# Kernel optimization log

Hardware: AMD Instinct MI355X
Metric: run time of the kernel (lower is better)

The kernel has to match this reference:

```python
import jax, jax.numpy as jnp
import numpy as np

B, L = 2, 1024
D_MODEL, D_CKV, D_CQ = 1024, 256, 512
N_HEAD, D_HEAD, D_ROPE = 8, 64, 32
N_IDX_HEAD = 4
K_TS, LW = 96, 64
ROPE_BASE = 10000.0


def setup_inputs() -> dict:
    key = jax.random.key(0)
    ks = jax.random.split(key, 14)
    def w(k, shape, fan_in):
        return jax.random.normal(k, shape, dtype=jnp.float32) * (fan_in ** -0.5)
    return {
        "x": jax.random.normal(ks[0], (B, L, D_MODEL), dtype=jnp.float32),
        "W_dkv": w(ks[1], (D_MODEL, D_CKV), D_MODEL),
        "W_uk": w(ks[2], (D_CKV, N_HEAD * D_HEAD), D_CKV),
        "W_uv": w(ks[3], (D_CKV, N_HEAD * D_HEAD), D_CKV),
        "W_dq": w(ks[4], (D_MODEL, D_CQ), D_MODEL),
        "W_uq": w(ks[5], (D_CQ, N_HEAD * D_HEAD), D_CQ),
        "W_qr": w(ks[6], (D_CQ, N_HEAD * D_ROPE), D_CQ),
        "W_kr": w(ks[7], (D_MODEL, D_ROPE), D_MODEL),
        "W_out": w(ks[8], (N_HEAD * D_HEAD, D_MODEL), N_HEAD * D_HEAD),
        "idx_wq": w(ks[9], (D_MODEL, N_IDX_HEAD * D_HEAD), D_MODEL),
        "idx_wk": w(ks[10], (D_MODEL, D_HEAD), D_MODEL),
        "idx_w": jnp.ones((N_IDX_HEAD,), dtype=jnp.float32),
        "raw_delta": jax.random.normal(ks[11], (D_ROPE // 2,), dtype=jnp.float32) * 0.1,
    }


def _pope(x, angles):
    # PoPE: softplus -> chunk in half -> rotate by (base_angle + learned delta)
    cos, sin = jnp.cos(angles), jnp.sin(angles)
    mu1, mu2 = jnp.split(jax.nn.softplus(x), 2, axis=-1)
    return jnp.concatenate([mu1 * cos - mu2 * sin, mu1 * sin + mu2 * cos], axis=-1)


def _forward(x, W_dkv, W_uk, W_uv, W_dq, W_uq, W_qr, W_kr, W_out,
             idx_wq, idx_wk, idx_w, raw_delta):
    B_, L_, _ = x.shape
    c_kv = x @ W_dkv                                    # [B,L,d_ckv]

    # ---- LightningIndexer ----
    q_i = (x @ idx_wq).reshape(B_, L_, N_IDX_HEAD, D_HEAD)
    k_i = x @ idx_wk                                    # [B,L,D_HEAD]
    s_i = jax.nn.relu(jnp.einsum('bthd,bsd->bths', q_i, k_i))
    I = jnp.einsum('bths,h->bts', s_i, idx_w)           # [B,L,L]

    # ---- TokenSelector (local window forced in, causal masked out, top-k) ----
    qpos = jnp.arange(L_)[:, None]
    kpos = jnp.arange(L_)[None, :]
    local = (kpos >= qpos - LW + 1) & (kpos <= qpos)
    causal = kpos > qpos
    I = jnp.where(local[None], jnp.inf, I)
    I = jnp.where(causal[None], -jnp.inf, I)
    kk = min(K_TS, L_)
    _, idx = jax.lax.top_k(I, kk)                       # [B,L,kk] int32

    bi = jnp.arange(B_)[:, None, None]
    # gather-after-project (per-token linear => identical math, far less memory)
    key_c = (c_kv @ W_uk)[bi, idx].reshape(B_, L_, kk, N_HEAD, D_HEAD)
    value = (c_kv @ W_uv)[bi, idx].reshape(B_, L_, kk, N_HEAD, D_HEAD)

    c_q = x @ W_dq                                      # [B,L,d_cq]
    query_c = (c_q @ W_uq).reshape(B_, L_, N_HEAD, D_HEAD)

    # ---- PoPE angles ----
    half = D_ROPE // 2
    theta = 1.0 / ROPE_BASE ** (2.0 * jnp.arange(half, dtype=jnp.float32) / D_ROPE)
    delta = -2.0 * jnp.pi * jax.nn.sigmoid(raw_delta)   # [half]
    angles_q = jnp.arange(L_, dtype=jnp.float32)[:, None] * theta[None, :] + delta  # [L,half]
    query_r = _pope((c_q @ W_qr).reshape(B_, L_, N_HEAD, D_ROPE),
                    angles_q[None, :, None, :])         # [B,L,H,D_ROPE]

    # key_r: PoPE applied along the selected-slot axis (faithful to original permute)
    kr_sel = (x @ W_kr)[bi, idx]                        # [B,L,kk,D_ROPE]
    angles_k = jnp.arange(kk, dtype=jnp.float32)[:, None] * theta[None, :] + delta  # [kk,half]
    key_r = _pope(kr_sel, angles_k[None, None, :, :])   # [B,L,kk,D_ROPE]

    # ---- per-query sparse attention ----
    scale = (D_HEAD + D_ROPE) ** (-0.5)
    q_c = query_c.transpose(0, 2, 1, 3)                 # [B,H,L,d]
    q_r = query_r.transpose(0, 2, 1, 3)                 # [B,H,L,dr]
    k_c = key_c.transpose(0, 3, 1, 2, 4)                # [B,H,L,kk,d]
    v = value.transpose(0, 3, 1, 2, 4)                  # [B,H,L,kk,d]
    scores = (jnp.einsum('bhld,bhlkd->bhlk', q_c, k_c)
              + jnp.einsum('bhld,blkd->bhlk', q_r, key_r)) * scale
    attn = jax.nn.softmax(scores.astype(jnp.float32), axis=-1).astype(v.dtype)
    out = jnp.einsum('bhlk,bhlkd->bhld', attn, v)       # [B,H,L,d]
    out = out.transpose(0, 2, 1, 3).reshape(B_, L_, N_HEAD * D_HEAD)
    return out @ W_out


def reference(x, W_dkv, W_uk, W_uv, W_dq, W_uq, W_qr, W_kr, W_out,
              idx_wq, idx_wk, idx_w, raw_delta):
    return _forward(x, W_dkv, W_uk, W_uv, W_dq, W_uq, W_qr, W_kr, W_out,
                    idx_wq, idx_wk, idx_w, raw_delta)
```

## Files before the change

### kernel.cpp

```cpp
#include <hip/hip_runtime.h>
#include <math.h>

typedef unsigned short u16;
typedef unsigned int u32;
typedef unsigned long long u64;
typedef _Float16 f16;
typedef __attribute__((ext_vector_type(8))) _Float16 f16x8;
typedef __attribute__((ext_vector_type(4))) float f32x4;

#define L      1024
#define NH     8
#define DH     64
#define DR     32
#define KTS    96
#define LWIN   64
#define NKV    1024
#define NQP    768

__device__ __forceinline__ float softplusf(float x) {
  return fmaxf(x, 0.f) + log1pf(expf(-fabsf(x)));
}
__device__ __forceinline__ f32x4 mf16(f16x8 a, f16x8 b, f32x4 c) {
  return __builtin_amdgcn_mfma_f32_16x16x32_f16(a, b, c, 0, 0, 0);
}
__device__ __forceinline__ u64 pack4(u16 a, u16 b, u16 c, u16 d) {
  return (u64)a | ((u64)b << 16) | ((u64)c << 32) | ((u64)d << 48);
}
__device__ __forceinline__ u64 umax64(u64 a, u64 b) { return a > b ? a : b; }
__device__ __forceinline__ void f16split(float x, u16& h, u16& l) {
  f16 hh = (f16)x;
  float r = x - (float)hh;
  f16 ll = (f16)r;
  h = *(u16*)&hh; l = *(u16*)&ll;
}
__device__ __forceinline__ u16 f16bits(float x) {
  f16 hh = (f16)x;
  return *(u16*)&hh;
}

struct TSrc { const float* p; int n0, w; };
struct WJob { TSrc s0, s1, s2, s3, s4; int K; u16 *Ph, *Pl; int nbx, nby; };

__global__ __launch_bounds__(256) void wsplit4(WJob j0, WJob j1, WJob j2,
                                               WJob j3) {
  __shared__ float tile[32][33];
  WJob j = (blockIdx.z == 0) ? j0
         : (blockIdx.z == 1) ? j1
         : (blockIdx.z == 2) ? j2 : j3;
  if ((int)blockIdx.x >= j.nbx || (int)blockIdx.y >= j.nby) return;
  const int k0 = blockIdx.y * 32, n0 = blockIdx.x * 32;
  const int tid = threadIdx.x;
  const float* sp = nullptr; int off = 0, w = 0;
  if (j.s0.p && n0 >= j.s0.n0 && n0 < j.s0.n0 + j.s0.w) { sp = j.s0.p; off = j.s0.n0; w = j.s0.w; }
  else if (j.s1.p && n0 >= j.s1.n0 && n0 < j.s1.n0 + j.s1.w) { sp = j.s1.p; off = j.s1.n0; w = j.s1.w; }
  else if (j.s2.p && n0 >= j.s2.n0 && n0 < j.s2.n0 + j.s2.w) { sp = j.s2.p; off = j.s2.n0; w = j.s2.w; }
  else if (j.s3.p && n0 >= j.s3.n0 && n0 < j.s3.n0 + j.s3.w) { sp = j.s3.p; off = j.s3.n0; w = j.s3.w; }
  else if (j.s4.p && n0 >= j.s4.n0 && n0 < j.s4.n0 + j.s4.w) { sp = j.s4.p; off = j.s4.n0; w = j.s4.w; }
  {
    const int kl = tid >> 3, n4 = (tid & 7) * 4;
    float4 v = make_float4(0.f, 0.f, 0.f, 0.f);
    if (sp) v = *(const float4*)(sp + (size_t)(k0 + kl) * w + (n0 - off) + n4);
    tile[kl][n4 + 0] = v.x; tile[kl][n4 + 1] = v.y;
    tile[kl][n4 + 2] = v.z; tile[kl][n4 + 3] = v.w;
  }
  __syncthreads();
  const int nl = tid >> 3, k4 = (tid & 7) * 4;
  u16 h[4], lo[4];
#pragma unroll
  for (int q = 0; q < 4; ++q) f16split(tile[k4 + q][nl], h[q], lo[q]);
  const size_t o = (size_t)(n0 + nl) * j.K + k0 + k4;
  *(u64*)(j.Ph + o) = pack4(h[0], h[1], h[2], h[3]);
  *(u64*)(j.Pl + o) = pack4(lo[0], lo[1], lo[2], lo[3]);
}

__global__ __launch_bounds__(256) void xsplit(
    const float* __restrict__ x, u16* __restrict__ Xh, u16* __restrict__ Xl) {
  const int i = (blockIdx.x * 256 + threadIdx.x) * 4;
  float4 v = *(const float4*)(x + i);
  float e[4] = {v.x, v.y, v.z, v.w};
  u16 h[4], lo[4];
#pragma unroll
  for (int j = 0; j < 4; ++j) f16split(e[j], h[j], lo[j]);
  *(u64*)(Xh + i) = pack4(h[0], h[1], h[2], h[3]);
  *(u64*)(Xl + i) = pack4(lo[0], lo[1], lo[2], lo[3]);
}

struct GArg {
  const u16 *A0, *A1, *B0, *B1;
  float* C; u16* Ch;
  u16 *Qh, *Ql, *Kh, *Kl; float* KR; const float* IW;
  int lda, ldc, K, nbn;
};

template <int NPROD, int OUT>
__device__ __forceinline__ void gemm_body(const GArg& g, u16* Al, u16* Bl) {
  const int NS = (NPROD == 1) ? 1 : 2;
  const int tid = threadIdx.x;
  const int l = tid & 63, w = tid >> 6;
  const int wr = w >> 1, wc = w & 1;
  const int l15 = l & 15, l4 = l >> 4;
  const int bm = blockIdx.y * 128, bn = blockIdx.x * 128;
  const int ar2 = tid >> 1, akc = (tid & 1) * 16;
  const int brr = tid >> 2, bkc = (tid & 3) * 8;

  f32x4 acc[4][4];
#pragma unroll
  for (int i = 0; i < 4; ++i)
#pragma unroll
    for (int j = 0; j < 4; ++j) acc[i][j] = (f32x4){0.f, 0.f, 0.f, 0.f};

  for (int k0 = 0; k0 < g.K; k0 += 32) {
#pragma unroll
    for (int p = 0; p < NS; ++p) {
      const u16* Ap = (p == 0) ? g.A0 : g.A1;
      const size_t ab = (size_t)(bm + ar2) * g.lda + k0 + akc;
      *(uint4*)&Al[p * 5120 + ar2 * 40 + akc] = *(const uint4*)(Ap + ab);
      *(uint4*)&Al[p * 5120 + ar2 * 40 + akc + 8] = *(const uint4*)(Ap + ab + 8);
      const u16* Bp = (p == 0) ? g.B0 : g.B1;
#pragma unroll
      for (int i = 0; i < 2; ++i) {
        const int row = brr + i * 64;
        *(uint4*)&Bl[p * 5120 + row * 40 + bkc] =
            *(const uint4*)(Bp + (size_t)(bn + row) * g.K + k0 + bkc);
      }
    }
    __syncthreads();
    f16x8 af[NS == 1 ? 1 : 2][4], bf[NS == 1 ? 1 : 2][4];
#pragma unroll
    for (int f = 0; f < 4; ++f) {
      const int arow = wr * 64 + f * 16 + l15;
      const int brow = wc * 64 + f * 16 + l15;
#pragma unroll
      for (int p = 0; p < NS; ++p) {
        af[p][f] = *(const f16x8*)&Al[p * 5120 + arow * 40 + l4 * 8];
        bf[p][f] = *(const f16x8*)&Bl[p * 5120 + brow * 40 + l4 * 8];
      }
    }
#pragma unroll
    for (int fm = 0; fm < 4; ++fm)
#pragma unroll
      for (int fn = 0; fn < 4; ++fn) {
        f32x4 c = acc[fm][fn];
        c = mf16(af[0][fm], bf[0][fn], c);
        if (NPROD == 3) {
          c = mf16(af[0][fm], bf[1][fn], c);
          c = mf16(af[1][fm], bf[0][fn], c);
        }
        acc[fm][fn] = c;
      }
    __syncthreads();
  }
  if (OUT == 3) {
    const float w0 = g.IW[0], w1 = g.IW[1], w2 = g.IW[2], w3 = g.IW[3];
#pragma unroll
    for (int fm = 0; fm < 4; ++fm) {
      const int tt = (bm >> 2) + wr * 16 + fm * 4 + l4;
#pragma unroll
      for (int fn = 0; fn < 4; ++fn) {
        const int col = bn + wc * 64 + fn * 16 + l15;
        const f32x4 a = acc[fm][fn];
        float v = w0 * fmaxf(a[0], 0.f) + w1 * fmaxf(a[1], 0.f)
                + w2 * fmaxf(a[2], 0.f) + w3 * fmaxf(a[3], 0.f);
        g.C[(size_t)tt * g.ldc + col] = v;
      }
    }
    return;
  }
#pragma unroll
  for (int fm = 0; fm < 4; ++fm)
#pragma unroll
    for (int j = 0; j < 4; ++j) {
      const int row = bm + wr * 64 + fm * 16 + l4 * 4 + j;
#pragma unroll
      for (int fn = 0; fn < 4; ++fn) {
        const int col = bn + wc * 64 + fn * 16 + l15;
        const float val = acc[fm][fn][j];
        if (OUT == 0) {
          g.C[(size_t)row * g.ldc + col] = val;
        } else if (OUT == 1) {
          g.Ch[(size_t)row * g.ldc + col] = f16bits(val);
        } else {
          u16 hh, ll;
          f16split(val, hh, ll);
          if (col < 256) {
            const size_t o = ((size_t)row * 4 + (col >> 6)) * 64 + (col & 63);
            g.Qh[o] = hh; g.Ql[o] = ll;
          } else if (col < 320) {
            const size_t o = (size_t)row * 64 + (col - 256);
            g.Kh[o] = hh; g.Kl[o] = ll;
          } else if (col < 352) {
            g.KR[(size_t)row * 32 + (col - 320)] = val;
          }
        }
      }
    }
}

template <int NPROD, int OUT>
__global__ __launch_bounds__(256) void mfma_gemm(GArg g0, GArg g1) {
  __shared__ u16 Al[(NPROD == 1 ? 1 : 2) * 5120];
  __shared__ u16 Bl[(NPROD == 1 ? 1 : 2) * 5120];
  GArg g = (blockIdx.z == 0) ? g0 : g1;
  if ((int)blockIdx.x >= g.nbn) return;
  gemm_body<NPROD, OUT>(g, Al, Bl);
}

__global__ __launch_bounds__(256) void g1_fused(GArg ga, GArg gb) {
  __shared__ u16 Al[2 * 5120];
  __shared__ u16 Bl[2 * 5120];
  if (blockIdx.z == 0) {
    if ((int)blockIdx.x >= ga.nbn) return;
    gemm_body<1, 1>(ga, Al, Bl);
  } else {
    if ((int)blockIdx.x >= gb.nbn) return;
    gemm_body<3, 2>(gb, Al, Bl);
  }
}

__global__ __launch_bounds__(256) void mid_fused(GArg gi0, GArg gi1, GArg g2,
                                                GArg g3) {
  __shared__ u16 Al[2 * 5120];
  __shared__ u16 Bl[2 * 5120];
  const int z = blockIdx.z;
  if (z < 2) {
    const GArg& g = z ? gi1 : gi0;
    if ((int)blockIdx.x >= g.nbn) return;
    gemm_body<3, 3>(g, Al, Bl);
  } else {
    const GArg& g = (z == 2) ? g2 : g3;
    if ((int)blockIdx.x >= g.nbn || (int)blockIdx.y >= 16) return;
    gemm_body<1, 0>(g, Al, Bl);
  }
}

__global__ __launch_bounds__(256) void topk2(
    const float* __restrict__ IM, int* __restrict__ idx_sel) {
  const int wave = threadIdx.x >> 6, lane = threadIdx.x & 63;
  const int bt = blockIdx.x * 4 + wave;
  const int b = bt >> 10, t = bt & 1023;
  int* out = idx_sel + (size_t)bt * KTS;
  if (t < LWIN) {
    out[lane] = lane;
    if (lane < 32) out[64 + lane] = 64 + lane;
    return;
  }
  out[lane] = t - 63 + lane;
  const int nf = t - 63;
  const float* Irow = IM + ((size_t)b << 20) + ((size_t)t << 10);
  u64 key[16];
#pragma unroll
  for (int gq = 0; gq < 4; ++gq) {
    const int s0 = gq * 256 + lane * 4;
    float4 v = make_float4(0.f, 0.f, 0.f, 0.f);
    if (s0 < nf) v = *(const float4*)(Irow + s0);
    float e[4] = {v.x, v.y, v.z, v.w};
#pragma unroll
    for (int c = 0; c < 4; ++c) {
      u64 k = 0ull;
      const int s = s0 + c;
      if (s < nf) {
        unsigned ib = __float_as_uint(e[c]);
        if (ib == 0x80000000u) ib = 0u;
        ib = (ib & 0x80000000u) ? ~ib : (ib | 0x80000000u);
        k = ((u64)ib << 32) | (u64)(0xFFFFFFFFu - (unsigned)s);
      }
      key[gq * 4 + c] = k;
    }
  }
  u64 lm = key[0];
#pragma unroll
  for (int j = 1; j < 16; ++j) lm = umax64(lm, key[j]);
  const int topM = nf < 32 ? nf : 32;
  for (int it = 0; it < topM; ++it) {
    u64 m = lm;
#pragma unroll
    for (int off = 32; off > 0; off >>= 1) m = umax64(m, __shfl_xor(m, off));
    if (lane == 0)
      out[64 + it] = (int)(0xFFFFFFFFu - (unsigned)(m & 0xFFFFFFFFull));
    if (lm == m) {
#pragma unroll
      for (int j = 0; j < 16; ++j)
        if (key[j] == m) key[j] = 0ull;
      lm = key[0];
#pragma unroll
      for (int j = 1; j < 16; ++j) lm = umax64(lm, key[j]);
    }
  }
  if (lane < 32 - topM) out[64 + topM + lane] = t + 1 + lane;
}

__global__ __launch_bounds__(256) void attn_kernel(
    const float* __restrict__ qproj, const float* __restrict__ kvproj,
    const float* __restrict__ krc, const int* __restrict__ idx_sel,
    const float* __restrict__ raw_delta, u16* __restrict__ aoh) {
  const int bt = ((blockIdx.x & 7) << 8) | (blockIdx.x >> 3);
  const int b = bt >> 10;
  const int t = bt & 1023;
  const int tid = threadIdx.x;

  __shared__ __align__(16) float qcs[NH * DH];
  __shared__ __align__(16) float qrs[NH * DR];
  __shared__ __align__(16) float krs[KTS * DR];
  __shared__ float scS[NH * 100];
  __shared__ int selS[KTS];
  __shared__ int offS[KTS];
  __shared__ float thetav[16], deltav[16];
  __shared__ float mu[NH * DR];

  const float* qrow = qproj + (size_t)bt * NQP;
  qcs[tid] = qrow[tid];
  qcs[256 + tid] = qrow[256 + tid];
  mu[tid] = softplusf(qrow[512 + tid]);
  if (tid < KTS) {
    int s = idx_sel[(size_t)bt * KTS + tid];
    selS[tid] = s;
    offS[tid] = s * NKV;
  }
  if (tid < 16) {
    thetav[tid] = (float)(1.0 / pow(10000.0, (double)tid / 16.0));
    float r = raw_delta[tid];
    deltav[tid] = -6.2831853071795864769f * (1.f / (1.f + expf(-r)));
  }
  __syncthreads();

  if (tid < 128) {
    int h = tid >> 4, i = tid & 15;
    float ang = (float)t * thetav[i] + deltav[i];
    float c = cosf(ang), s = sinf(ang);
    float m1 = mu[h * DR + i], m2 = mu[h * DR + 16 + i];
    qrs[h * DR + i] = m1 * c - m2 * s;
    qrs[h * DR + 16 + i] = m1 * s + m2 * c;
  }
  const float* krb = krc + (size_t)b * L * 32;
  for (int e = tid; e < KTS * 16; e += 256) {
    int k = e >> 4, i = e & 15;
    int s = selS[k];
    float x1 = krb[(size_t)s * 32 + i];
    float x2 = krb[(size_t)s * 32 + 16 + i];
    float m1 = softplusf(x1), m2 = softplusf(x2);
    float ang = (float)k * thetav[i] + deltav[i];
    float c = cosf(ang), sn = sinf(ang);
    krs[k * DR + i] = m1 * c - m2 * sn;
    krs[k * DR + 16 + i] = m1 * sn + m2 * c;
  }
  __syncthreads();

  const float scale = 0.10206207261596575f;
  const int h = tid >> 5;
  const int l = tid & 31;
  const float2 qv = *(const float2*)&qcs[h * DH + 2 * l];
  const float qr1 = qrs[h * DR + l];
  const float* kvb = kvproj + (size_t)b * L * NKV;
#pragma unroll 8
  for (int k = 0; k < KTS; ++k) {
    const float2 kv = *(const float2*)(kvb + offS[k] + 2 * tid);
    float p = qv.x * kv.x + qv.y * kv.y + qr1 * krs[k * DR + l];
#pragma unroll
    for (int off = 16; off > 0; off >>= 1) p += __shfl_xor(p, off, 32);
    if (l == 0) scS[h * 100 + k] = p * scale;
  }
  __syncthreads();

  {
    float s0 = scS[h * 100 + l], s1 = scS[h * 100 + l + 32],
          s2 = scS[h * 100 + l + 64];
    float mx = fmaxf(fmaxf(s0, s1), s2);
#pragma unroll
    for (int off = 16; off > 0; off >>= 1) mx = fmaxf(mx, __shfl_xor(mx, off, 32));
    float e0 = expf(s0 - mx), e1 = expf(s1 - mx), e2 = expf(s2 - mx);
    float sum = e0 + e1 + e2;
#pragma unroll
    for (int off = 16; off > 0; off >>= 1) sum += __shfl_xor(sum, off, 32);
    float inv = 1.f / sum;
    scS[h * 100 + l] = e0 * inv;
    scS[h * 100 + l + 32] = e1 * inv;
    scS[h * 100 + l + 64] = e2 * inv;
  }
  __syncthreads();

  float2 acc = make_float2(0.f, 0.f);
#pragma unroll 4
  for (int k = 0; k < KTS; ++k) {
    const float2 v = *(const float2*)(kvb + offS[k] + 512 + 2 * tid);
    const float w = scS[h * 100 + k];
    acc.x += w * v.x;
    acc.y += w * v.y;
  }
  const size_t o = (size_t)bt * 512 + 2 * tid;
  *(u32*)(aoh + o) = (u32)f16bits(acc.x) | ((u32)f16bits(acc.y) << 16);
}

extern "C" void kernel_launch(void* const* d_in, const int* in_sizes, int n_in,
                              void* d_out, int out_size, void* d_ws, size_t ws_size,
                              hipStream_t stream) {
  const float* x      = (const float*)d_in[0];
  const float* W_dkv  = (const float*)d_in[1];
  const float* W_uk   = (const float*)d_in[2];
  const float* W_uv   = (const float*)d_in[3];
  const float* W_dq   = (const float*)d_in[4];
  const float* W_uq   = (const float*)d_in[5];
  const float* W_qr   = (const float*)d_in[6];
  const float* W_kr   = (const float*)d_in[7];
  const float* W_out  = (const float*)d_in[8];
  const float* idx_wq = (const float*)d_in[9];
  const float* idx_wk = (const float*)d_in[10];
  const float* idx_w  = (const float*)d_in[11];
  const float* raw_dl = (const float*)d_in[12];
  float* out = (float*)d_out;

  const int M = 2 * L;
  u16* BxT_h  = (u16*)d_ws;
  u16* BxT_l  = BxT_h + 1152 * 1024;
  u16* BkvT_h = BxT_l + 1152 * 1024;
  u16* BkvT_l = BkvT_h + 1024 * 256;
  u16* BqT_h  = BkvT_l + 1024 * 256;
  u16* BqT_l  = BqT_h + 768 * 512;
  u16* WoT_h  = BqT_l + 768 * 512;
  u16* WoT_l  = WoT_h + 1024 * 512;
  u16* Xh     = WoT_l + 1024 * 512;
  u16* Xl     = Xh + (size_t)M * 1024;
  u16* XPh    = Xl + (size_t)M * 1024;
  u16* AOh    = XPh + (size_t)M * 768;
  u16* Qih    = AOh + (size_t)M * 512;
  u16* Qil    = Qih + (size_t)M * 4 * 64;
  u16* Kih    = Qil + (size_t)M * 4 * 64;
  u16* Kil    = Kih + (size_t)M * 64;
  float* krc    = (float*)(Kil + (size_t)M * 64);
  float* kvproj = krc + (size_t)M * 32;
  float* qproj  = kvproj + (size_t)M * NKV;
  int* sel      = (int*)(qproj + (size_t)M * NQP);
  float* IM     = (float*)Xh;

  dim3 blk(256);
  TSrc z = {nullptr, 0, 0};
  GArg Z = {};
  {
    WJob j0 = {{W_dkv, 0, 256}, {W_dq, 256, 512}, {idx_wq, 768, 256},
               {idx_wk, 1024, 64}, {W_kr, 1088, 32},
               1024, BxT_h, BxT_l, 36, 32};
    WJob j1 = {{W_uk, 0, 512}, {W_uv, 512, 512}, z, z, z,
               256, BkvT_h, BkvT_l, 32, 8};
    WJob j2 = {{W_uq, 0, 512}, {W_qr, 512, 256}, z, z, z,
               512, BqT_h, BqT_l, 24, 16};
    WJob j3 = {{W_out, 0, 1024}, z, z, z, z,
               512, WoT_h, WoT_l, 32, 16};
    hipLaunchKernelGGL(wsplit4, dim3(36, 32, 4), blk, 0, stream, j0, j1, j2, j3);
  }
  hipLaunchKernelGGL(xsplit, dim3(M * 1024 / (256 * 4)), blk, 0, stream,
                     x, Xh, Xl);
  {
    GArg ga = Z;
    ga.A0 = Xh; ga.B0 = BxT_h;
    ga.Ch = XPh; ga.lda = 1024; ga.ldc = 768; ga.K = 1024; ga.nbn = 6;
    GArg gb = Z;
    gb.A0 = Xh; gb.A1 = Xl;
    gb.B0 = BxT_h + 768 * 1024; gb.B1 = BxT_l + 768 * 1024;
    gb.Qh = Qih; gb.Ql = Qil; gb.Kh = Kih; gb.Kl = Kil; gb.KR = krc;
    gb.lda = 1024; gb.ldc = 0; gb.K = 1024; gb.nbn = 3;
    hipLaunchKernelGGL(g1_fused, dim3(6, M / 128, 2), blk, 0, stream, ga, gb);
  }
  {
    GArg gi0 = Z, gi1 = Z, g2 = Z, g3 = Z;
    gi0.A0 = Qih; gi0.A1 = Qil; gi0.B0 = Kih; gi0.B1 = Kil;
    gi0.C = IM; gi0.IW = idx_w;
    gi0.lda = 64; gi0.ldc = 1024; gi0.K = 64; gi0.nbn = 8;
    gi1 = gi0;
    gi1.A0 = Qih + 4096 * 64; gi1.A1 = Qil + 4096 * 64;
    gi1.B0 = Kih + 1024 * 64; gi1.B1 = Kil + 1024 * 64;
    gi1.C = IM + 1024 * 1024;
    g2.A0 = XPh; g2.B0 = BkvT_h;
    g2.C = kvproj; g2.lda = 768; g2.ldc = 1024; g2.K = 256; g2.nbn = 8;
    g3.A0 = XPh + 256; g3.B0 = BqT_h;
    g3.C = qproj; g3.lda = 768; g3.ldc = 768; g3.K = 512; g3.nbn = 6;
    hipLaunchKernelGGL(mid_fused, dim3(8, 32, 4), blk, 0, stream,
                       gi0, gi1, g2, g3);
  }
  hipLaunchKernelGGL(topk2, dim3(M / 4), blk, 0, stream, IM, sel);
  hipLaunchKernelGGL(attn_kernel, dim3(M), blk, 0, stream,
                     qproj, kvproj, krc, sel, raw_dl, AOh);
  {
    GArg g = Z;
    g.A0 = AOh; g.B0 = WoT_h;
    g.C = out; g.lda = 512; g.ldc = 1024; g.K = 512; g.nbn = 8;
    hipLaunchKernelGGL((mfma_gemm<1, 0>), dim3(8, M / 128, 1), blk, 0, stream,
                       g, g);
  }
}
```

Baseline: 283.8 us.

## Store attention keys in fp16 and use packed dot2 with batched shuffle reduction

The kv projection GEMM now writes the key half as fp16 and the value half as fp32 into separate buffers. The attention kernel gathers fp16 keys, which halves the bytes per selected key, and computes the score with the fdot2 instruction. The shuffle reduction now handles four keys at once through a butterfly transpose, cutting the number of shuffles per key. The cost is reduced key precision (fp16 queries and keys) in the score computation.

```diff
diff --git a/kernel.cpp b/kernel.cpp
--- a/kernel.cpp
+++ b/kernel.cpp
@@ -5,6 +5,7 @@
 typedef unsigned int u32;
 typedef unsigned long long u64;
 typedef _Float16 f16;
+typedef __attribute__((ext_vector_type(2))) _Float16 f16x2;
 typedef __attribute__((ext_vector_type(8))) _Float16 f16x8;
 typedef __attribute__((ext_vector_type(4))) float f32x4;
 
@@ -14,7 +15,6 @@
 #define DR     32
 #define KTS    96
 #define LWIN   64
-#define NKV    1024
 #define NQP    768
 
 __device__ __forceinline__ float softplusf(float x) {
@@ -36,6 +36,11 @@
 __device__ __forceinline__ u16 f16bits(float x) {
   f16 hh = (f16)x;
   return *(u16*)&hh;
+}
+__device__ __forceinline__ float fdot2u(u32 a, u32 b, float c) {
+  union { u32 u; f16x2 h; } ua, ub;
+  ua.u = a; ub.u = b;
+  return __builtin_amdgcn_fdot2(ua.h, ub.h, c, false);
 }
 
 struct TSrc { const float* p; int n0, w; };
@@ -179,6 +184,9 @@
           g.C[(size_t)row * g.ldc + col] = val;
         } else if (OUT == 1) {
           g.Ch[(size_t)row * g.ldc + col] = f16bits(val);
+        } else if (OUT == 4) {
+          if (col < 512) g.Ch[(size_t)row * 512 + col] = f16bits(val);
+          else g.C[(size_t)row * 512 + (col - 512)] = val;
         } else {
           u16 hh, ll;
           f16split(val, hh, ll);
@@ -226,10 +234,12 @@
     const GArg& g = z ? gi1 : gi0;
     if ((int)blockIdx.x >= g.nbn) return;
     gemm_body<3, 3>(g, Al, Bl);
+  } else if (z == 2) {
+    if ((int)blockIdx.x >= g2.nbn || (int)blockIdx.y >= 16) return;
+    gemm_body<1, 4>(g2, Al, Bl);
   } else {
-    const GArg& g = (z == 2) ? g2 : g3;
-    if ((int)blockIdx.x >= g.nbn || (int)blockIdx.y >= 16) return;
-    gemm_body<1, 0>(g, Al, Bl);
+    if ((int)blockIdx.x >= g3.nbn || (int)blockIdx.y >= 16) return;
+    gemm_body<1, 0>(g3, Al, Bl);
   }
 }
 
@@ -290,17 +300,18 @@
 }
 
 __global__ __launch_bounds__(256) void attn_kernel(
-    const float* __restrict__ qproj, const float* __restrict__ kvproj,
-    const float* __restrict__ krc, const int* __restrict__ idx_sel,
-    const float* __restrict__ raw_delta, u16* __restrict__ aoh) {
+    const float* __restrict__ qproj, const u16* __restrict__ kcf,
+    const float* __restrict__ vc, const float* __restrict__ krc,
+    const int* __restrict__ idx_sel, const float* __restrict__ raw_delta,
+    u16* __restrict__ aoh) {
   const int bt = ((blockIdx.x & 7) << 8) | (blockIdx.x >> 3);
   const int b = bt >> 10;
   const int t = bt & 1023;
   const int tid = threadIdx.x;
 
-  __shared__ __align__(16) float qcs[NH * DH];
   __shared__ __align__(16) float qrs[NH * DR];
   __shared__ __align__(16) float krs[KTS * DR];
+  __shared__ u32 qc2S[256];
   __shared__ float scS[NH * 100];
   __shared__ int selS[KTS];
   __shared__ int offS[KTS];
@@ -308,13 +319,16 @@
   __shared__ float mu[NH * DR];
 
   const float* qrow = qproj + (size_t)bt * NQP;
-  qcs[tid] = qrow[tid];
-  qcs[256 + tid] = qrow[256 + tid];
+  {
+    const int hh = tid >> 5, ll = tid & 31;
+    float q0 = qrow[hh * 64 + 2 * ll], q1 = qrow[hh * 64 + 2 * ll + 1];
+    qc2S[tid] = (u32)f16bits(q0) | ((u32)f16bits(q1) << 16);
+  }
   mu[tid] = softplusf(qrow[512 + tid]);
   if (tid < KTS) {
     int s = idx_sel[(size_t)bt * KTS + tid];
     selS[tid] = s;
-    offS[tid] = s * NKV;
+    offS[tid] = s * 512;
   }
   if (tid < 16) {
     thetav[tid] = (float)(1.0 / pow(10000.0, (double)tid / 16.0));
@@ -348,16 +362,30 @@
   const float scale = 0.10206207261596575f;
   const int h = tid >> 5;
   const int l = tid & 31;
-  const float2 qv = *(const float2*)&qcs[h * DH + 2 * l];
+  const u32 q2 = qc2S[tid];
   const float qr1 = qrs[h * DR + l];
-  const float* kvb = kvproj + (size_t)b * L * NKV;
-#pragma unroll 8
-  for (int k = 0; k < KTS; ++k) {
-    const float2 kv = *(const float2*)(kvb + offS[k] + 2 * tid);
-    float p = qv.x * kv.x + qv.y * kv.y + qr1 * krs[k * DR + l];
-#pragma unroll
-    for (int off = 16; off > 0; off >>= 1) p += __shfl_xor(p, off, 32);
-    if (l == 0) scS[h * 100 + k] = p * scale;
+  const u16* kcb = kcf + (size_t)b * L * 512 + h * 64 + 2 * l;
+  const float* vcb = vc + (size_t)b * L * 512;
+
+#pragma unroll 4
+  for (int i = 0; i < KTS / 4; ++i) {
+    const int kb = i * 4;
+    u32 kv0 = *(const u32*)(kcb + offS[kb + 0]);
+    u32 kv1 = *(const u32*)(kcb + offS[kb + 1]);
+    u32 kv2 = *(const u32*)(kcb + offS[kb + 2]);
+    u32 kv3 = *(const u32*)(kcb + offS[kb + 3]);
+    float p0 = fdot2u(q2, kv0, qr1 * krs[(kb + 0) * DR + l]);
+    float p1 = fdot2u(q2, kv1, qr1 * krs[(kb + 1) * DR + l]);
+    float p2 = fdot2u(q2, kv2, qr1 * krs[(kb + 2) * DR + l]);
+    float p3 = fdot2u(q2, kv3, qr1 * krs[(kb + 3) * DR + l]);
+    float a = ((l & 16) ? p1 : p0) + __shfl_xor((l & 16) ? p0 : p1, 16, 32);
+    float bb = ((l & 16) ? p3 : p2) + __shfl_xor((l & 16) ? p2 : p3, 16, 32);
+    float c = ((l & 8) ? bb : a) + __shfl_xor((l & 8) ? a : bb, 8, 32);
+    c += __shfl_xor(c, 4, 32);
+    c += __shfl_xor(c, 2, 32);
+    c += __shfl_xor(c, 1, 32);
+    if ((l & 7) == 0)
+      scS[h * 100 + kb + ((l >> 4) & 1) + ((l >> 3) & 1) * 2] = c * scale;
   }
   __syncthreads();
 
@@ -381,7 +409,7 @@
   float2 acc = make_float2(0.f, 0.f);
 #pragma unroll 4
   for (int k = 0; k < KTS; ++k) {
-    const float2 v = *(const float2*)(kvb + offS[k] + 512 + 2 * tid);
+    const float2 v = *(const float2*)(vcb + offS[k] + 2 * tid);
     const float w = scS[h * 100 + k];
     acc.x += w * v.x;
     acc.y += w * v.y;
@@ -425,9 +453,10 @@
   u16* Qil    = Qih + (size_t)M * 4 * 64;
   u16* Kih    = Qil + (size_t)M * 4 * 64;
   u16* Kil    = Kih + (size_t)M * 64;
-  float* krc    = (float*)(Kil + (size_t)M * 64);
-  float* kvproj = krc + (size_t)M * 32;
-  float* qproj  = kvproj + (size_t)M * NKV;
+  u16* kcf    = Kil + (size_t)M * 64;
+  float* krc    = (float*)(kcf + (size_t)M * 512);
+  float* vc     = krc + (size_t)M * 32;
+  float* qproj  = vc + (size_t)M * 512;
   int* sel      = (int*)(qproj + (size_t)M * NQP);
   float* IM     = (float*)Xh;
 
@@ -469,7 +498,7 @@
     gi1.B0 = Kih + 1024 * 64; gi1.B1 = Kil + 1024 * 64;
     gi1.C = IM + 1024 * 1024;
     g2.A0 = XPh; g2.B0 = BkvT_h;
-    g2.C = kvproj; g2.lda = 768; g2.ldc = 1024; g2.K = 256; g2.nbn = 8;
+    g2.C = vc; g2.Ch = kcf; g2.lda = 768; g2.ldc = 512; g2.K = 256; g2.nbn = 8;
     g3.A0 = XPh + 256; g3.B0 = BqT_h;
     g3.C = qproj; g3.lda = 768; g3.ldc = 768; g3.K = 512; g3.nbn = 6;
     hipLaunchKernelGGL(mid_fused, dim3(8, 32, 4), blk, 0, stream,
@@ -477,7 +506,7 @@
   }
   hipLaunchKernelGGL(topk2, dim3(M / 4), blk, 0, stream, IM, sel);
   hipLaunchKernelGGL(attn_kernel, dim3(M), blk, 0, stream,
-                     qproj, kvproj, krc, sel, raw_dl, AOh);
+                     qproj, kcf, vc, krc, sel, raw_dl, AOh);
   {
     GArg g = Z;
     g.A0 = AOh; g.B0 = WoT_h;
```

Result: faster. 247.8 us (-12.7%).
